# Optimization experiments

Hardware: AMD Instinct MI355X
Metric: run time of the kernel (lower is better)

The kernel has to match this reference:

```python
import jax, jax.numpy as jnp
import numpy as np

# DoG parameters derived from init kwargs: sigma_low=1.0, truncate=4.0
SIGMA_LOW = 1.0
SIGMA_HIGH = 1.6  # sigma_low * 1.6
KSIZE_LOW = 9     # 2*ceil(4.0*1.0)+1
KSIZE_HIGH = 15   # 2*ceil(4.0*1.6)+1


def gaussian_kernel1d(ksize: int, sigma: float) -> jnp.ndarray:
    # Matches kornia's 1D gaussian: centered, normalized to sum 1.
    t = jnp.arange(ksize, dtype=jnp.float32) - (ksize - 1) / 2.0
    g = jnp.exp(-(t * t) / (2.0 * sigma * sigma))
    return g / jnp.sum(g)


def _conv1d_along_axis(x: jnp.ndarray, g: jnp.ndarray, axis: int) -> jnp.ndarray:
    # x: (B, C, D, H, W); depthwise 1D cross-correlation along `axis` with
    # replicate ('edge') boundary handling, as in kornia filter3d(border_type='replicate').
    C = x.shape[1]
    k = g.shape[0]
    pads = [(0, 0)] * 5
    pads[axis] = (k // 2, k // 2)
    xp = jnp.pad(x, pads, mode='edge')
    kshape = [1, 1, 1]
    kshape[axis - 2] = k
    w = jnp.tile(g.reshape(1, 1, *kshape), (C, 1, 1, 1, 1))  # (C,1,kd,kh,kw)
    return jax.lax.conv_general_dilated(
        xp, w, window_strides=(1, 1, 1), padding='VALID',
        dimension_numbers=('NCDHW', 'OIDHW', 'NCDHW'),
        feature_group_count=C)


def gaussian_blur3d(x: jnp.ndarray, sigma: float, ksize: int) -> jnp.ndarray:
    # The 3D kernel is an outer product of normalized 1D gaussians, so the
    # dense 3D convolution is exactly equal to three separable 1D passes.
    g = gaussian_kernel1d(ksize, sigma)
    for ax in (2, 3, 4):
        x = _conv1d_along_axis(x, g, ax)
    return x


def setup_inputs() -> dict:
    key = jax.random.key(0)
    x = jax.random.normal(key, (2, 1, 160, 160, 160), dtype=jnp.float32)
    return {"x": x}


def reference(x) -> jnp.ndarray:
    low_pass = gaussian_blur3d(x, SIGMA_LOW, KSIZE_LOW)
    high_pass = gaussian_blur3d(x, SIGMA_HIGH, KSIZE_HIGH)
    return low_pass - high_pass
```

## Files before the change

kernel.cpp:

```cpp
#include <hip/hip_runtime.h>
#include <math.h>

#define DIMS 160
#define PLANE (DIMS*DIMS)
#define NB 2
#define RH 7
#define RL 4
#define KH 15
#define KL 9
#define TSX 16
#define TSY 32
#define NTX (DIMS/TSX)
#define NTY (DIMS/TSY)
#define CZ 16
#define NCH (DIMS/CZ)
#define NSTEPS (CZ + 2*RH)
#define YHR (TSY + 2*RH)
#define SR 48
#define SH 50
#define SL 42
#define RAWSZ (YHR*SR)
#define XHSZ (TSX*SH)
#define XLSZ (TSX*SL)
#define NBLK (NTX*NTY*NCH*NB)

struct DoGW { float gl[KL]; float gh[KH]; };

__global__ __launch_bounds__(512, 4)
void dog_v11(const float* __restrict__ X, float* __restrict__ out, DoGW w) {
  __shared__ __align__(16) float sRaw[2][RAWSZ];
  __shared__ __align__(16) float sXh[2][XHSZ];
  __shared__ __align__(16) float sXl[2][XLSZ];

  const int bid = blockIdx.x;
  const int xt = bid % NTX;
  const int yt = (bid / NTX) % NTY;
  const int zc = (bid / (NTX * NTY)) % NCH;
  const int b  = bid / (NTX * NTY * NCH);
  const int x0 = xt * TSX, y0 = yt * TSY, z0 = zc * CZ;
  const float* Xb = X + (size_t)b * DIMS * PLANE;
  const int tid = threadIdx.x;
  const bool xfast = (x0 >= 8) && (x0 + 24 <= DIMS);

  const bool y_on = tid < 256;
  const int cx  = tid & 15;
  const int cy0 = 2 * ((tid >> 4) & 15);
  const int hb = cx * SH + cy0;
  const int lb = cx * SL + cy0;
  float* const obase = out + ((size_t)b * DIMS * PLANE) + (size_t)(y0 + cy0) * DIMS + (x0 + cx);

  const bool x_on = (tid >= 256) && (tid < 256 + YHR * 4);
  const int xu = tid - 256;
  const int xr = xu >> 2, xq = xu & 3;

  const bool l_on = tid >= (512 - YHR * 4);
  const int lu = tid - (512 - YHR * 4);
  const int lrow = lu >> 2, lt = lu & 3;
  const int lyg = min(max(y0 + lrow - RH, 0), DIMS - 1);
  const int lxb = x0 - 8 + 4 * lt;

  float4 vA, vB;

  auto loadP = [&](int s) {
    const int zsrc = min(max(z0 - RH + s, 0), DIMS - 1);
    const float* rowp = Xb + ((size_t)zsrc * DIMS + lyg) * DIMS;
    if (xfast) {
      vA = *(const float4*)(rowp + lxb);
      vB = *(const float4*)(rowp + lxb + 16);
    } else {
      vA.x = rowp[min(max(lxb + 0, 0), DIMS - 1)];
      vA.y = rowp[min(max(lxb + 1, 0), DIMS - 1)];
      vA.z = rowp[min(max(lxb + 2, 0), DIMS - 1)];
      vA.w = rowp[min(max(lxb + 3, 0), DIMS - 1)];
      vB.x = rowp[min(max(lxb + 16, 0), DIMS - 1)];
      vB.y = rowp[min(max(lxb + 17, 0), DIMS - 1)];
      vB.z = rowp[min(max(lxb + 18, 0), DIMS - 1)];
      vB.w = rowp[min(max(lxb + 19, 0), DIMS - 1)];
    }
  };
  auto stageP = [&](int buf) {
    float* p = &sRaw[buf][lrow * SR + 4 * lt];
    *(float4*)(p) = vA;
    *(float4*)(p + 16) = vB;
  };

  float D0[KH], D1[KH];
  #pragma unroll
  for (int i = 0; i < KH; ++i) { D0[i] = 0.f; D1[i] = 0.f; }

  auto consumeQ = [&](int q) {
    const int qb = q & 1;
    float f[16], g[10];
    #pragma unroll
    for (int j = 0; j < 8; ++j) {
      float2 t = *(const float2*)&sXh[qb][hb + 2 * j];
      f[2 * j] = t.x; f[2 * j + 1] = t.y;
    }
    #pragma unroll
    for (int j = 0; j < 5; ++j) {
      float2 t = *(const float2*)&sXl[qb][lb + 2 * j];
      g[2 * j] = t.x; g[2 * j + 1] = t.y;
    }
    float ph0 = 0.f, ph1 = 0.f, pl0 = 0.f, pl1 = 0.f;
    #pragma unroll
    for (int j = 0; j < KH; ++j) {
      ph0 = fmaf(w.gh[j], f[j], ph0);
      ph1 = fmaf(w.gh[j], f[j + 1], ph1);
    }
    #pragma unroll
    for (int j = 0; j < KL; ++j) {
      pl0 = fmaf(w.gl[j], g[j], pl0);
      pl1 = fmaf(w.gl[j], g[j + 1], pl1);
    }
    #pragma unroll
    for (int i = 0; i < KH; ++i) {
      D0[i] = fmaf(-w.gh[KH - 1 - i], ph0, D0[i]);
      D1[i] = fmaf(-w.gh[KH - 1 - i], ph1, D1[i]);
    }
    #pragma unroll
    for (int i = 3; i < KL + 3; ++i) {
      D0[i] = fmaf(w.gl[KL + 2 - i], pl0, D0[i]);
      D1[i] = fmaf(w.gl[KL + 2 - i], pl1, D1[i]);
    }
    if (q >= 2 * RH) {
      float* op = obase + (size_t)(z0 + q - 2 * RH) * PLANE;
      op[0]    = D0[0];
      op[DIMS] = D1[0];
    }
    #pragma unroll
    for (int i = 0; i < KH - 1; ++i) { D0[i] = D0[i + 1]; D1[i] = D1[i + 1]; }
    D0[KH - 1] = 0.f; D1[KH - 1] = 0.f;
  };

  auto xconvP = [&](int cur) {
    const float* p = &sRaw[cur][xr * SR + 4 * xq];
    float v[20];
    #pragma unroll
    for (int j = 0; j < 5; ++j) {
      float4 t = *(const float4*)(p + 4 * j);
      v[4 * j] = t.x; v[4 * j + 1] = t.y; v[4 * j + 2] = t.z; v[4 * j + 3] = t.w;
    }
    #pragma unroll
    for (int c = 0; c < 4; ++c) {
      float a = 0.f;
      #pragma unroll
      for (int k = 0; k < KH; ++k) a = fmaf(w.gh[k], v[c + 1 + k], a);
      sXh[cur][(4 * xq + c) * SH + xr] = a;
    }
    if (xr >= 3 && xr <= 42) {
      #pragma unroll
      for (int c = 0; c < 4; ++c) {
        float a = 0.f;
        #pragma unroll
        for (int k = 0; k < KL; ++k) a = fmaf(w.gl[k], v[c + 4 + k], a);
        sXl[cur][(4 * xq + c) * SL + (xr - 3)] = a;
      }
    }
  };

  if (l_on) { loadP(0); stageP(0); loadP(1); }
  __syncthreads();

  #pragma unroll 5
  for (int s = 0; s < NSTEPS; ++s) {
    const int cur = s & 1;
    if (l_on) {
      if (s + 1 < NSTEPS) stageP(1 - cur);
      if (s + 2 < NSTEPS) loadP(s + 2);
    }
    if (y_on && s >= 1) consumeQ(s - 1);
    if (x_on) xconvP(cur);
    __syncthreads();
  }
  if (y_on) consumeQ(NSTEPS - 1);
}

extern "C" void kernel_launch(void* const* d_in, const int* in_sizes, int n_in,
                              void* d_out, int out_size, void* d_ws, size_t ws_size,
                              hipStream_t stream) {
  const float* X = (const float*)d_in[0];
  float* out = (float*)d_out;

  DoGW w;
  {
    double s = 0.0;
    for (int i = 0; i < KL; ++i) {
      double t = i - (KL - 1) / 2.0;
      double g = exp(-(t * t) / (2.0 * 1.0 * 1.0));
      w.gl[i] = (float)g; s += g;
    }
    for (int i = 0; i < KL; ++i) w.gl[i] = (float)((double)w.gl[i] / s);
    s = 0.0;
    for (int i = 0; i < KH; ++i) {
      double t = i - (KH - 1) / 2.0;
      double g = exp(-(t * t) / (2.0 * 1.6 * 1.6));
      w.gh[i] = (float)g; s += g;
    }
    for (int i = 0; i < KH; ++i) w.gh[i] = (float)((double)w.gh[i] / s);
  }

  dog_v11<<<NBLK, 512, 0, stream>>>(X, out, w);
}
```

Baseline: 139.2 us.

## Load raw rows directly into x-conv registers, drop staging smem, double z-chunk

Removes the raw-input shared-memory staging buffer and the dedicated loader threads. The x-convolution threads now fetch their own 20-wide row segments from global memory into double-buffered registers, one step ahead, which drops the block to 448 threads. The z-chunk is also doubled to amortize the 14-plane halo recompute. In exchange each x thread reads more from global memory, register pressure rises, and there are half as many blocks.

```diff
diff --git a/kernel.cpp b/kernel.cpp
--- a/kernel.cpp
+++ b/kernel.cpp
@@ -12,23 +12,21 @@
 #define TSY 32
 #define NTX (DIMS/TSX)
 #define NTY (DIMS/TSY)
-#define CZ 16
+#define CZ 32
 #define NCH (DIMS/CZ)
 #define NSTEPS (CZ + 2*RH)
 #define YHR (TSY + 2*RH)
-#define SR 48
 #define SH 50
 #define SL 42
-#define RAWSZ (YHR*SR)
 #define XHSZ (TSX*SH)
 #define XLSZ (TSX*SL)
+#define NTHREADS 448
 #define NBLK (NTX*NTY*NCH*NB)
 
 struct DoGW { float gl[KL]; float gh[KH]; };
 
-__global__ __launch_bounds__(512, 4)
-void dog_v11(const float* __restrict__ X, float* __restrict__ out, DoGW w) {
-  __shared__ __align__(16) float sRaw[2][RAWSZ];
+__global__ __launch_bounds__(NTHREADS, 4)
+void dog_v12(const float* __restrict__ X, float* __restrict__ out, DoGW w) {
   __shared__ __align__(16) float sXh[2][XHSZ];
   __shared__ __align__(16) float sXl[2][XLSZ];
 
@@ -40,7 +38,6 @@
   const int x0 = xt * TSX, y0 = yt * TSY, z0 = zc * CZ;
   const float* Xb = X + (size_t)b * DIMS * PLANE;
   const int tid = threadIdx.x;
-  const bool xfast = (x0 >= 8) && (x0 + 24 <= DIMS);
 
   const bool y_on = tid < 256;
   const int cx  = tid & 15;
@@ -52,36 +49,51 @@
   const bool x_on = (tid >= 256) && (tid < 256 + YHR * 4);
   const int xu = tid - 256;
   const int xr = xu >> 2, xq = xu & 3;
+  const int xyg = min(max(y0 + xr - RH, 0), DIMS - 1);
+  const int gx0 = x0 - 8 + 4 * xq;
+  const bool tfast = (gx0 >= 0) && (gx0 + 20 <= DIMS);
 
-  const bool l_on = tid >= (512 - YHR * 4);
-  const int lu = tid - (512 - YHR * 4);
-  const int lrow = lu >> 2, lt = lu & 3;
-  const int lyg = min(max(y0 + lrow - RH, 0), DIMS - 1);
-  const int lxb = x0 - 8 + 4 * lt;
+  float4 PA[5], PB[5];
 
-  float4 vA, vB;
-
-  auto loadP = [&](int s) {
+  auto issueLoad = [&](int s, float4 (&P)[5]) {
     const int zsrc = min(max(z0 - RH + s, 0), DIMS - 1);
-    const float* rowp = Xb + ((size_t)zsrc * DIMS + lyg) * DIMS;
-    if (xfast) {
-      vA = *(const float4*)(rowp + lxb);
-      vB = *(const float4*)(rowp + lxb + 16);
+    const float* rp = Xb + ((size_t)zsrc * DIMS + xyg) * DIMS;
+    if (tfast) {
+      #pragma unroll
+      for (int j = 0; j < 5; ++j) P[j] = *(const float4*)(rp + gx0 + 4 * j);
     } else {
-      vA.x = rowp[min(max(lxb + 0, 0), DIMS - 1)];
-      vA.y = rowp[min(max(lxb + 1, 0), DIMS - 1)];
-      vA.z = rowp[min(max(lxb + 2, 0), DIMS - 1)];
-      vA.w = rowp[min(max(lxb + 3, 0), DIMS - 1)];
-      vB.x = rowp[min(max(lxb + 16, 0), DIMS - 1)];
-      vB.y = rowp[min(max(lxb + 17, 0), DIMS - 1)];
-      vB.z = rowp[min(max(lxb + 18, 0), DIMS - 1)];
-      vB.w = rowp[min(max(lxb + 19, 0), DIMS - 1)];
+      #pragma unroll
+      for (int j = 0; j < 5; ++j) {
+        P[j].x = rp[min(max(gx0 + 4 * j + 0, 0), DIMS - 1)];
+        P[j].y = rp[min(max(gx0 + 4 * j + 1, 0), DIMS - 1)];
+        P[j].z = rp[min(max(gx0 + 4 * j + 2, 0), DIMS - 1)];
+        P[j].w = rp[min(max(gx0 + 4 * j + 3, 0), DIMS - 1)];
+      }
     }
   };
-  auto stageP = [&](int buf) {
-    float* p = &sRaw[buf][lrow * SR + 4 * lt];
-    *(float4*)(p) = vA;
-    *(float4*)(p + 16) = vB;
+
+  auto xcompute = [&](int cur, const float4 (&P)[5]) {
+    float v[20];
+    #pragma unroll
+    for (int j = 0; j < 5; ++j) {
+      v[4 * j] = P[j].x; v[4 * j + 1] = P[j].y; v[4 * j + 2] = P[j].z; v[4 * j + 3] = P[j].w;
+    }
+    #pragma unroll
+    for (int c = 0; c < 4; ++c) {
+      float a = 0.f;
+      #pragma unroll
+      for (int k = 0; k < KH; ++k) a = fmaf(w.gh[k], v[c + 1 + k], a);
+      sXh[cur][(4 * xq + c) * SH + xr] = a;
+    }
+    if (xr >= 3 && xr <= 42) {
+      #pragma unroll
+      for (int c = 0; c < 4; ++c) {
+        float a = 0.f;
+        #pragma unroll
+        for (int k = 0; k < KL; ++k) a = fmaf(w.gl[k], v[c + 4 + k], a);
+        sXl[cur][(4 * xq + c) * SL + (xr - 3)] = a;
+      }
+    }
   };
 
   float D0[KH], D1[KH];
@@ -132,45 +144,18 @@
     D0[KH - 1] = 0.f; D1[KH - 1] = 0.f;
   };
 
-  auto xconvP = [&](int cur) {
-    const float* p = &sRaw[cur][xr * SR + 4 * xq];
-    float v[20];
-    #pragma unroll
-    for (int j = 0; j < 5; ++j) {
-      float4 t = *(const float4*)(p + 4 * j);
-      v[4 * j] = t.x; v[4 * j + 1] = t.y; v[4 * j + 2] = t.z; v[4 * j + 3] = t.w;
-    }
-    #pragma unroll
-    for (int c = 0; c < 4; ++c) {
-      float a = 0.f;
-      #pragma unroll
-      for (int k = 0; k < KH; ++k) a = fmaf(w.gh[k], v[c + 1 + k], a);
-      sXh[cur][(4 * xq + c) * SH + xr] = a;
-    }
-    if (xr >= 3 && xr <= 42) {
-      #pragma unroll
-      for (int c = 0; c < 4; ++c) {
-        float a = 0.f;
-        #pragma unroll
-        for (int k = 0; k < KL; ++k) a = fmaf(w.gl[k], v[c + 4 + k], a);
-        sXl[cur][(4 * xq + c) * SL + (xr - 3)] = a;
-      }
-    }
+  auto seg = [&](int s, const float4 (&Prd)[5], float4 (&Pwr)[5]) {
+    if (x_on && s + 1 < NSTEPS) issueLoad(s + 1, Pwr);
+    if (y_on && s >= 1) consumeQ(s - 1);
+    if (x_on) xcompute(s & 1, Prd);
+    __syncthreads();
   };
 
-  if (l_on) { loadP(0); stageP(0); loadP(1); }
-  __syncthreads();
+  if (x_on) issueLoad(0, PA);
 
-  #pragma unroll 5
-  for (int s = 0; s < NSTEPS; ++s) {
-    const int cur = s & 1;
-    if (l_on) {
-      if (s + 1 < NSTEPS) stageP(1 - cur);
-      if (s + 2 < NSTEPS) loadP(s + 2);
-    }
-    if (y_on && s >= 1) consumeQ(s - 1);
-    if (x_on) xconvP(cur);
-    __syncthreads();
+  for (int sp = 0; sp < NSTEPS; sp += 2) {
+    seg(sp,     PA, PB);
+    seg(sp + 1, PB, PA);
   }
   if (y_on) consumeQ(NSTEPS - 1);
 }
@@ -199,5 +184,5 @@
     for (int i = 0; i < KH; ++i) w.gh[i] = (float)((double)w.gh[i] / s);
   }
 
-  dog_v11<<<NBLK, 512, 0, stream>>>(X, out, w);
+  dog_v12<<<NBLK, NTHREADS, 0, stream>>>(X, out, w);
 }
```

Measured after the change: 155.9 us. +12.0%, slower.

## Double z-chunk depth and process two z-planes per barrier step

Applied to the files above, without the earlier changes.

Raises the z-chunk from 16 to 32 planes, which lowers the share of redundant halo planes each block loads and convolves. The shared-memory staging buffers gain a second slot so each loop iteration loads, x-convolves and consumes two z-planes, halving the number of __syncthreads barriers. In exchange, shared memory and live registers per block roughly double and the grid shrinks to half as many blocks, which may reduce occupancy and latency hiding.

```diff
diff --git a/kernel.cpp b/kernel.cpp
--- a/kernel.cpp
+++ b/kernel.cpp
@@ -12,9 +12,10 @@
 #define TSY 32
 #define NTX (DIMS/TSX)
 #define NTY (DIMS/TSY)
-#define CZ 16
+#define CZ 32
 #define NCH (DIMS/CZ)
 #define NSTEPS (CZ + 2*RH)
+#define NSEG (NSTEPS/2)
 #define YHR (TSY + 2*RH)
 #define SR 48
 #define SH 50
@@ -27,10 +28,10 @@
 struct DoGW { float gl[KL]; float gh[KH]; };
 
 __global__ __launch_bounds__(512, 4)
-void dog_v11(const float* __restrict__ X, float* __restrict__ out, DoGW w) {
-  __shared__ __align__(16) float sRaw[2][RAWSZ];
-  __shared__ __align__(16) float sXh[2][XHSZ];
-  __shared__ __align__(16) float sXl[2][XLSZ];
+void dog_v13(const float* __restrict__ X, float* __restrict__ out, DoGW w) {
+  __shared__ __align__(16) float sRaw[2][2][RAWSZ];
+  __shared__ __align__(16) float sXh[2][2][XHSZ];
+  __shared__ __align__(16) float sXl[2][2][XLSZ];
 
   const int bid = blockIdx.x;
   const int xt = bid % NTX;
@@ -59,9 +60,9 @@
   const int lyg = min(max(y0 + lrow - RH, 0), DIMS - 1);
   const int lxb = x0 - 8 + 4 * lt;
 
-  float4 vA, vB;
-
-  auto loadP = [&](int s) {
+  float4 a0, b0, a1, b1;
+
+  auto loadP = [&](int s, float4& vA, float4& vB) {
     const int zsrc = min(max(z0 - RH + s, 0), DIMS - 1);
     const float* rowp = Xb + ((size_t)zsrc * DIMS + lyg) * DIMS;
     if (xfast) {
@@ -78,8 +79,8 @@
       vB.w = rowp[min(max(lxb + 19, 0), DIMS - 1)];
     }
   };
-  auto stageP = [&](int buf) {
-    float* p = &sRaw[buf][lrow * SR + 4 * lt];
+  auto stageP = [&](int buf, int slot, const float4& vA, const float4& vB) {
+    float* p = &sRaw[buf][slot][lrow * SR + 4 * lt];
     *(float4*)(p) = vA;
     *(float4*)(p + 16) = vB;
   };
@@ -88,17 +89,16 @@
   #pragma unroll
   for (int i = 0; i < KH; ++i) { D0[i] = 0.f; D1[i] = 0.f; }
 
-  auto consumeQ = [&](int q) {
-    const int qb = q & 1;
+  auto consumeQ = [&](int q, const float* __restrict__ sh, const float* __restrict__ sl) {
     float f[16], g[10];
     #pragma unroll
     for (int j = 0; j < 8; ++j) {
-      float2 t = *(const float2*)&sXh[qb][hb + 2 * j];
+      float2 t = *(const float2*)&sh[hb + 2 * j];
       f[2 * j] = t.x; f[2 * j + 1] = t.y;
     }
     #pragma unroll
     for (int j = 0; j < 5; ++j) {
-      float2 t = *(const float2*)&sXl[qb][lb + 2 * j];
+      float2 t = *(const float2*)&sl[lb + 2 * j];
       g[2 * j] = t.x; g[2 * j + 1] = t.y;
     }
     float ph0 = 0.f, ph1 = 0.f, pl0 = 0.f, pl1 = 0.f;
@@ -132,8 +132,8 @@
     D0[KH - 1] = 0.f; D1[KH - 1] = 0.f;
   };
 
-  auto xconvP = [&](int cur) {
-    const float* p = &sRaw[cur][xr * SR + 4 * xq];
+  auto xconvP = [&](int cur, int slot) {
+    const float* p = &sRaw[cur][slot][xr * SR + 4 * xq];
     float v[20];
     #pragma unroll
     for (int j = 0; j < 5; ++j) {
@@ -145,7 +145,7 @@
       float a = 0.f;
       #pragma unroll
       for (int k = 0; k < KH; ++k) a = fmaf(w.gh[k], v[c + 1 + k], a);
-      sXh[cur][(4 * xq + c) * SH + xr] = a;
+      sXh[cur][slot][(4 * xq + c) * SH + xr] = a;
     }
     if (xr >= 3 && xr <= 42) {
       #pragma unroll
@@ -153,26 +153,44 @@
         float a = 0.f;
         #pragma unroll
         for (int k = 0; k < KL; ++k) a = fmaf(w.gl[k], v[c + 4 + k], a);
-        sXl[cur][(4 * xq + c) * SL + (xr - 3)] = a;
+        sXl[cur][slot][(4 * xq + c) * SL + (xr - 3)] = a;
       }
     }
   };
 
-  if (l_on) { loadP(0); stageP(0); loadP(1); }
+  if (l_on) {
+    loadP(0, a0, b0); loadP(1, a1, b1);
+    stageP(0, 0, a0, b0); stageP(0, 1, a1, b1);
+    loadP(2, a0, b0); loadP(3, a1, b1);
+  }
   __syncthreads();
 
-  #pragma unroll 5
-  for (int s = 0; s < NSTEPS; ++s) {
-    const int cur = s & 1;
+  for (int k = 0; k < NSEG; ++k) {
+    const int cur = k & 1;
     if (l_on) {
-      if (s + 1 < NSTEPS) stageP(1 - cur);
-      if (s + 2 < NSTEPS) loadP(s + 2);
-    }
-    if (y_on && s >= 1) consumeQ(s - 1);
-    if (x_on) xconvP(cur);
+      if (2 * k + 2 < NSTEPS) {
+        stageP(1 - cur, 0, a0, b0);
+        stageP(1 - cur, 1, a1, b1);
+      }
+      if (2 * k + 4 < NSTEPS) {
+        loadP(2 * k + 4, a0, b0);
+        loadP(2 * k + 5, a1, b1);
+      }
+    }
+    if (y_on && k >= 1) {
+      consumeQ(2 * k - 2, &sXh[1 - cur][0][0], &sXl[1 - cur][0][0]);
+      consumeQ(2 * k - 1, &sXh[1 - cur][1][0], &sXl[1 - cur][1][0]);
+    }
+    if (x_on) {
+      xconvP(cur, 0);
+      xconvP(cur, 1);
+    }
     __syncthreads();
   }
-  if (y_on) consumeQ(NSTEPS - 1);
+  if (y_on) {
+    consumeQ(NSTEPS - 2, &sXh[0][0][0], &sXl[0][0][0]);
+    consumeQ(NSTEPS - 1, &sXh[0][1][0], &sXl[0][1][0]);
+  }
 }
 
 extern "C" void kernel_launch(void* const* d_in, const int* in_sizes, int n_in,
@@ -199,5 +217,5 @@
     for (int i = 0; i < KH; ++i) w.gh[i] = (float)((double)w.gh[i] / s);
   }
 
-  dog_v11<<<NBLK, 512, 0, stream>>>(X, out, w);
+  dog_v13<<<NBLK, 512, 0, stream>>>(X, out, w);
 }
```

Measured after the change: 129.6 us. -6.9%, faster.

## Split DoG into XY-plane kernel and Z-streaming kernel via workspace

Applied to the files above, without the earlier changes.

Replaces the single fused z-streaming kernel with two kernels when enough workspace is available. The first computes the x and y passes per z-plane for both sigmas into two full-volume workspace buffers, and the second streams along z per column to apply the z pass and the difference. This avoids recomputing the halo x/y convolutions for every z-chunk and removes the in-loop synchronisation. In exchange it writes and re-reads about 4x the input volume through global memory. The fallback kernel's z-chunk size is also doubled.

```diff
diff --git a/kernel.cpp b/kernel.cpp
--- a/kernel.cpp
+++ b/kernel.cpp
@@ -3,16 +3,175 @@
 
 #define DIMS 160
 #define PLANE (DIMS*DIMS)
+#define VOL (DIMS*PLANE)
 #define NB 2
 #define RH 7
 #define RL 4
 #define KH 15
 #define KL 9
+
+struct DoGW { float gl[KL]; float gh[KH]; };
+
+
+#define A_TS 32
+#define A_RR 46
+#define A_SRAW 48
+#define A_SH 50
+#define A_SL 42
+
+__global__ __launch_bounds__(256, 4)
+void dog_xy(const float* __restrict__ X, float* __restrict__ wsH,
+            float* __restrict__ wsL, DoGW w) {
+  __shared__ __align__(16) float sRaw[A_RR * A_SRAW];
+  __shared__ __align__(16) float sHx[A_TS * A_SH];
+  __shared__ __align__(16) float sLx[A_TS * A_SL];
+
+  const int bid = blockIdx.x;
+  const int xt = bid % 5, yt = (bid / 5) % 5, zp = bid / 25;
+  const int x0 = xt * A_TS, y0 = yt * A_TS;
+  const float* P = X + (size_t)zp * PLANE;
+  const int tid = threadIdx.x;
+  const bool xin = (xt > 0) && (xt < 4);
+
+  #pragma unroll
+  for (int rr = 0; rr < 3; ++rr) {
+    const int u = tid + rr * 256;
+    if (u < A_RR * 12) {
+      const int row = u / 12, q = u % 12;
+      const int yg = min(max(y0 + row - RH, 0), DIMS - 1);
+      const float* rp = P + (size_t)yg * DIMS;
+      const int gx = x0 - 8 + 4 * q;
+      float4 v;
+      if (xin || (gx >= 0 && gx + 4 <= DIMS)) {
+        v = *(const float4*)(rp + gx);
+      } else {
+        v.x = rp[min(max(gx + 0, 0), DIMS - 1)];
+        v.y = rp[min(max(gx + 1, 0), DIMS - 1)];
+        v.z = rp[min(max(gx + 2, 0), DIMS - 1)];
+        v.w = rp[min(max(gx + 3, 0), DIMS - 1)];
+      }
+      *(float4*)&sRaw[row * A_SRAW + 4 * q] = v;
+    }
+  }
+  __syncthreads();
+
+  #pragma unroll
+  for (int rr = 0; rr < 2; ++rr) {
+    const int u = tid + rr * 256;
+    if (u < A_RR * 8) {
+      const int row = u >> 3, q = u & 7;
+      const float* p = &sRaw[row * A_SRAW + 4 * q];
+      float v[20];
+      #pragma unroll
+      for (int j = 0; j < 5; ++j) {
+        float4 t = *(const float4*)(p + 4 * j);
+        v[4*j] = t.x; v[4*j+1] = t.y; v[4*j+2] = t.z; v[4*j+3] = t.w;
+      }
+      #pragma unroll
+      for (int c = 0; c < 4; ++c) {
+        float a = 0.f;
+        #pragma unroll
+        for (int k = 0; k < KH; ++k) a = fmaf(w.gh[k], v[c + 1 + k], a);
+        sHx[(4 * q + c) * A_SH + row] = a;
+      }
+      if (row >= 3 && row <= 42) {
+        #pragma unroll
+        for (int c = 0; c < 4; ++c) {
+          float a = 0.f;
+          #pragma unroll
+          for (int k = 0; k < KL; ++k) a = fmaf(w.gl[k], v[c + 4 + k], a);
+          sLx[(4 * q + c) * A_SL + (row - 3)] = a;
+        }
+      }
+    }
+  }
+  __syncthreads();
+
+  float* const oH = wsH + (size_t)zp * PLANE;
+  float* const oL = wsL + (size_t)zp * PLANE;
+  #pragma unroll
+  for (int rr = 0; rr < 2; ++rr) {
+    const int u = tid + rr * 256;
+    const int cx = u & 31, cy0 = 2 * ((u >> 5) & 15);
+    float f[16], g[10];
+    #pragma unroll
+    for (int j = 0; j < 8; ++j) {
+      float2 t = *(const float2*)&sHx[cx * A_SH + cy0 + 2 * j];
+      f[2*j] = t.x; f[2*j+1] = t.y;
+    }
+    #pragma unroll
+    for (int j = 0; j < 5; ++j) {
+      float2 t = *(const float2*)&sLx[cx * A_SL + cy0 + 2 * j];
+      g[2*j] = t.x; g[2*j+1] = t.y;
+    }
+    float ph0 = 0.f, ph1 = 0.f, pl0 = 0.f, pl1 = 0.f;
+    #pragma unroll
+    for (int j = 0; j < KH; ++j) {
+      ph0 = fmaf(w.gh[j], f[j], ph0);
+      ph1 = fmaf(w.gh[j], f[j + 1], ph1);
+    }
+    #pragma unroll
+    for (int j = 0; j < KL; ++j) {
+      pl0 = fmaf(w.gl[j], g[j], pl0);
+      pl1 = fmaf(w.gl[j], g[j + 1], pl1);
+    }
+    const int o = (y0 + cy0) * DIMS + x0 + cx;
+    oH[o] = ph0; oH[o + DIMS] = ph1;
+    oL[o] = pl0; oL[o + DIMS] = pl1;
+  }
+}
+
+#define B_CZ 40
+#define B_NP (B_CZ + 2*RH)
+
+__global__ __launch_bounds__(256, 4)
+void dog_z(const float* __restrict__ wsH, const float* __restrict__ wsL,
+           float* __restrict__ out, DoGW w) {
+  const int bid = blockIdx.x;
+  const int cb = bid % 200, zc = bid / 200;
+  const int col = cb * 256 + threadIdx.x;
+  const int b = col / PLANE, rem = col % PLANE;
+  const int zb = zc * B_CZ;
+  const float* __restrict__ pH = wsH + (size_t)b * VOL + rem;
+  const float* __restrict__ pL = wsL + (size_t)b * VOL + rem;
+  float* __restrict__ po = out + (size_t)b * VOL + rem;
+
+  auto ldH = [&](int q) -> float {
+    const int zs = min(max(zb - RH + q, 0), DIMS - 1);
+    return pH[(size_t)zs * PLANE];
+  };
+  auto ldL = [&](int q) -> float {
+    const int zs = min(max(zb - RH + q, 0), DIMS - 1);
+    return pL[(size_t)zs * PLANE];
+  };
+
+  float D[KH];
+  #pragma unroll
+  for (int i = 0; i < KH; ++i) D[i] = 0.f;
+
+  float hA = ldH(0), lA = ldL(0);
+  float hB = ldH(1), lB = ldL(1);
+  #pragma unroll 6
+  for (int q = 0; q < B_NP; ++q) {
+    float hC = 0.f, lC = 0.f;
+    if (q + 2 < B_NP) { hC = ldH(q + 2); lC = ldL(q + 2); }
+    #pragma unroll
+    for (int i = 0; i < KH; ++i) D[i] = fmaf(-w.gh[KH - 1 - i], hA, D[i]);
+    #pragma unroll
+    for (int i = 3; i < KL + 3; ++i) D[i] = fmaf(w.gl[KL + 2 - i], lA, D[i]);
+    if (q >= 2 * RH) po[(size_t)(zb + q - 2 * RH) * PLANE] = D[0];
+    #pragma unroll
+    for (int i = 0; i < KH - 1; ++i) D[i] = D[i + 1];
+    D[KH - 1] = 0.f;
+    hA = hB; lA = lB; hB = hC; lB = lC;
+  }
+}
+
 #define TSX 16
 #define TSY 32
 #define NTX (DIMS/TSX)
 #define NTY (DIMS/TSY)
-#define CZ 16
+#define CZ 32
 #define NCH (DIMS/CZ)
 #define NSTEPS (CZ + 2*RH)
 #define YHR (TSY + 2*RH)
@@ -24,10 +183,8 @@
 #define XLSZ (TSX*SL)
 #define NBLK (NTX*NTY*NCH*NB)
 
-struct DoGW { float gl[KL]; float gh[KH]; };
-
 __global__ __launch_bounds__(512, 4)
-void dog_v11(const float* __restrict__ X, float* __restrict__ out, DoGW w) {
+void dog_fb(const float* __restrict__ X, float* __restrict__ out, DoGW w) {
   __shared__ __align__(16) float sRaw[2][RAWSZ];
   __shared__ __align__(16) float sXh[2][XHSZ];
   __shared__ __align__(16) float sXl[2][XLSZ];
@@ -38,7 +195,7 @@
   const int zc = (bid / (NTX * NTY)) % NCH;
   const int b  = bid / (NTX * NTY * NCH);
   const int x0 = xt * TSX, y0 = yt * TSY, z0 = zc * CZ;
-  const float* Xb = X + (size_t)b * DIMS * PLANE;
+  const float* Xb = X + (size_t)b * VOL;
   const int tid = threadIdx.x;
   const bool xfast = (x0 >= 8) && (x0 + 24 <= DIMS);
 
@@ -47,7 +204,7 @@
   const int cy0 = 2 * ((tid >> 4) & 15);
   const int hb = cx * SH + cy0;
   const int lb = cx * SL + cy0;
-  float* const obase = out + ((size_t)b * DIMS * PLANE) + (size_t)(y0 + cy0) * DIMS + (x0 + cx);
+  float* const obase = out + (size_t)b * VOL + (size_t)(y0 + cy0) * DIMS + (x0 + cx);
 
   const bool x_on = (tid >= 256) && (tid < 256 + YHR * 4);
   const int xu = tid - 256;
@@ -60,7 +217,6 @@
   const int lxb = x0 - 8 + 4 * lt;
 
   float4 vA, vB;
-
   auto loadP = [&](int s) {
     const int zsrc = min(max(z0 - RH + s, 0), DIMS - 1);
     const float* rowp = Xb + ((size_t)zsrc * DIMS + lyg) * DIMS;
@@ -199,5 +355,13 @@
     for (int i = 0; i < KH; ++i) w.gh[i] = (float)((double)w.gh[i] / s);
   }
 
-  dog_v11<<<NBLK, 512, 0, stream>>>(X, out, w);
+  const size_t need = 2ull * NB * VOL * sizeof(float);
+  if (ws_size >= need) {
+    float* wsH = (float*)d_ws;
+    float* wsL = wsH + (size_t)NB * VOL;
+    dog_xy<<<NB * DIMS * 25, 256, 0, stream>>>(X, wsH, wsL, w);
+    dog_z<<<(NB * PLANE / 256) * (DIMS / B_CZ), 256, 0, stream>>>(wsH, wsL, out, w);
+  } else {
+    dog_fb<<<NBLK, 512, 0, stream>>>(X, out, w);
+  }
 }
```

Result: faster. 124.0 us (-10.9%).
